# Performance work log

Hardware: AMD Instinct MI355X
Metric: run time of the kernel (lower is better)

Reference implementation:

```python
import jax, jax.numpy as jnp
import numpy as np

B, S, H, DH, DM = 1024, 32, 32, 32, 1024  # seq==heads==head_dim==32 forced by module's reshapes


def setup_inputs() -> dict:
    key = jax.random.key(0)
    k1, k2 = jax.random.split(key)
    x = jax.random.normal(k1, (B, S, DM), dtype=jnp.float32)
    mask = jnp.ones((1, 1, S, DH), dtype=bool)
    W_qkv = jax.random.normal(k2, (DM, 3 * H * DH), dtype=jnp.float32) / np.sqrt(DM).astype(np.float32)
    return {"x": x, "mask": mask, "W_qkv": W_qkv}


def _rope(t, sin, cos):
    # t: [B, S, H, DH]; sin/cos: [S] broadcast over the HEADS axis (axis 2), as in the original
    t1, t2 = jnp.split(t, 2, axis=-1)
    rot = jnp.concatenate([-t2, t1], axis=-1)
    return t * cos.reshape(1, 1, -1, 1) + rot * sin.reshape(1, 1, -1, 1)


def reference(x, mask, W_qkv):
    b, seq_len, _ = x.shape
    qkv = x @ W_qkv  # [B, S, 3*H*DH]
    q, k, v = jnp.split(qkv, 3, axis=-1)
    q = q.reshape(b, -1, H, DH)
    k = k.reshape(b, -1, H, DH)
    v = v.reshape(b, -1, H, DH)
    pos = jnp.arange(seq_len, dtype=x.dtype)
    sin, cos = jnp.sin(pos), jnp.cos(pos)
    q = _rope(q, sin, cos)
    k = _rope(k, sin, cos)
    # matmul over heads axis (faithful to original): [B,S,H,DH] @ [B,S,DH,H] -> [B,S,H,H]
    attn = jnp.matmul(q, k.transpose(0, 1, 3, 2)) / jnp.sqrt(jnp.asarray(DH, x.dtype))
    attn = attn.reshape(b, H, seq_len, DH)  # valid only because H == 32
    attn = jnp.where(jnp.broadcast_to(mask, attn.shape), attn, -jnp.inf)
    attn = jax.nn.softmax(attn, axis=-1)
    out = jnp.matmul(attn, v)  # [B,H,S,DH] @ [B,S,H,DH]; batched since S==H==32
    return out.reshape(-1, seq_len, H * DH)
```

## Files before the change

### kernel.cpp

```cpp
#include <hip/hip_runtime.h>

typedef __bf16 bf16_t;
typedef __bf16 bf16x4 __attribute__((ext_vector_type(4)));
typedef __bf16 bf16x8 __attribute__((ext_vector_type(8)));
typedef float f32x4 __attribute__((ext_vector_type(4)));
typedef float f32x16 __attribute__((ext_vector_type(16)));
typedef unsigned int uint4v __attribute__((ext_vector_type(4)));

#define M_TOT 32768
#define N_TOT 3072
#define K_TOT 1024

#define WT_BYTES (3072u * 1024u * 2u)
#define XB_BYTES ((size_t)M_TOT * 1024 * 2)

#define SLOT 32768

__device__ __forceinline__ void gload_lds16(const void* g, void* l) {
  __builtin_amdgcn_global_load_lds(
      (const __attribute__((address_space(1))) unsigned int*)g,
      (__attribute__((address_space(3))) unsigned int*)l, 16, 0, 0);
}

__device__ __forceinline__ unsigned pk2(float a, float b) {
  unsigned short lo = __builtin_bit_cast(unsigned short, (bf16_t)a);
  unsigned short hi = __builtin_bit_cast(unsigned short, (bf16_t)b);
  return ((unsigned)hi << 16) | (unsigned)lo;
}

__global__ __launch_bounds__(256) void k_wt(const float* __restrict__ W,
                                            bf16_t* __restrict__ wt) {
  __shared__ float tile[64][65];
  const int c0 = blockIdx.x * 64, k0 = blockIdx.y * 64;
  const int t = threadIdx.x;
  for (int rep = 0; rep < 16; ++rep) {
    int lin = rep * 256 + t;
    int kl = lin >> 6, cl = lin & 63;
    tile[kl][cl] = W[(size_t)(k0 + kl) * 3072 + (c0 + cl)];
  }
  __syncthreads();
  const float scale = 0.17677669529663687f;
  for (int rep = 0; rep < 16; ++rep) {
    int lin = rep * 256 + t;
    int cl = lin >> 6, kl = lin & 63;
    int c = c0 + cl;
    float val;
    if (c < 2048) {
      int cc = c & 1023;
      int h = cc >> 5, d = cc & 31;
      float cv = cosf((float)h), sv = sinf((float)h);
      int clp = cl + ((d < 16) ? 16 : -16);
      float other = tile[kl][clp];
      val = tile[kl][cl] * cv + ((d < 16) ? -other : other) * sv;
      if (c < 1024) val *= scale;
    } else {
      val = tile[kl][cl];
    }
    wt[(size_t)c * 1024 + (k0 + kl)] = (bf16_t)val;
  }
}

__global__ __launch_bounds__(256) void k_xb(const float* __restrict__ x,
                                            bf16_t* __restrict__ xb) {
  const size_t nf4 = (size_t)M_TOT * K_TOT / 4;
  const float4* src = (const float4*)x;
  for (size_t i = (size_t)blockIdx.x * 256 + threadIdx.x; i < nf4;
       i += (size_t)gridDim.x * 256) {
    float4 a = src[i];
    bf16x4 o;
    o[0] = (bf16_t)a.x; o[1] = (bf16_t)a.y; o[2] = (bf16_t)a.z; o[3] = (bf16_t)a.w;
    *(bf16x4*)(&xb[i * 4]) = o;
  }
}

template <int STAGE, int VM>
__device__ __forceinline__ void ktile(const char* sR, char* sW,
                                      const char* src, int dstOff,
                                      int aoff, int boff,
                                      f32x4 (&acc)[8][4]) {
  if constexpr (STAGE) {
#pragma unroll
    for (int c = 0; c < 4; ++c)
      gload_lds16(src + c * 32768, sW + dstOff + c * 1024);
  }
  bf16x8 a[8], b[4];
#pragma unroll
  for (int m = 0; m < 4; ++m) a[m] = *(const bf16x8*)(sR + aoff + m * 2048);
  b[0] = *(const bf16x8*)(sR + boff);
  b[1] = *(const bf16x8*)(sR + boff + 4096);
  __builtin_amdgcn_sched_barrier(0);
  b[2] = *(const bf16x8*)(sR + boff + 8192);
  b[3] = *(const bf16x8*)(sR + boff + 12288);
  __builtin_amdgcn_sched_barrier(0);
#pragma unroll
  for (int m = 4; m < 8; ++m) a[m] = *(const bf16x8*)(sR + aoff + m * 2048);
  __builtin_amdgcn_sched_barrier(0);

  asm volatile("s_waitcnt lgkmcnt(6)" ::: "memory");
  __builtin_amdgcn_sched_barrier(0);
  __builtin_amdgcn_s_setprio(1);
#pragma unroll
  for (int m = 0; m < 4; ++m)
#pragma unroll
    for (int n = 0; n < 2; ++n)
      acc[m][n] = __builtin_amdgcn_mfma_f32_16x16x32_bf16(a[m], b[n], acc[m][n], 0, 0, 0);
  __builtin_amdgcn_s_setprio(0);

  asm volatile("s_waitcnt lgkmcnt(4)" ::: "memory");
  __builtin_amdgcn_sched_barrier(0);
  __builtin_amdgcn_s_setprio(1);
#pragma unroll
  for (int m = 0; m < 4; ++m)
#pragma unroll
    for (int n = 2; n < 4; ++n)
      acc[m][n] = __builtin_amdgcn_mfma_f32_16x16x32_bf16(a[m], b[n], acc[m][n], 0, 0, 0);
  __builtin_amdgcn_s_setprio(0);

  asm volatile("s_waitcnt lgkmcnt(0)" ::: "memory");
  __builtin_amdgcn_sched_barrier(0);
  __builtin_amdgcn_s_setprio(1);
#pragma unroll
  for (int m = 4; m < 8; ++m)
#pragma unroll
    for (int n = 2; n < 4; ++n)
      acc[m][n] = __builtin_amdgcn_mfma_f32_16x16x32_bf16(a[m], b[n], acc[m][n], 0, 0, 0);
#pragma unroll
  for (int m = 4; m < 8; ++m)
#pragma unroll
    for (int n = 0; n < 2; ++n)
      acc[m][n] = __builtin_amdgcn_mfma_f32_16x16x32_bf16(a[m], b[n], acc[m][n], 0, 0, 0);
  __builtin_amdgcn_s_setprio(0);

  if constexpr (VM == 4) asm volatile("s_waitcnt vmcnt(4)" ::: "memory");
  else if constexpr (VM == 0) asm volatile("s_waitcnt vmcnt(0)" ::: "memory");
  if constexpr (VM >= 0) __builtin_amdgcn_s_barrier();
}

__global__ __launch_bounds__(512, 2) void k_gemm(const bf16_t* __restrict__ xb,
                                                 const bf16_t* __restrict__ wt,
                                                 bf16_t* __restrict__ qk,
                                                 bf16_t* __restrict__ vb) {
  __shared__ __attribute__((aligned(16))) char lds[3 * SLOT];
  const int tid = threadIdx.x;
  const int w = tid >> 6, lane = tid & 63;
  const int wr = w >> 2, wc = w & 3;

  const int bid = blockIdx.x;
  const int swz = (bid & 7) * 192 + (bid >> 3);
  const int tm = swz / 12, tn = swz % 12;
  const int row0 = tm * 256, col0 = tn * 256;

  const int isB = w >> 2;
  const int rL = (w & 3) * 64 + (lane >> 2);
  const int g = (lane & 3) ^ ((lane >> 3) & 3);
  const char* src = isB
      ? (const char*)wt + (size_t)(col0 + rL) * 2048 + g * 16
      : (const char*)xb + (size_t)(row0 + rL) * 2048 + g * 16;
  const int dstOff = (w & 3) * 4096 + isB * 16384;

  const int rsel = lane & 15;
  const int kx = (((lane >> 4) ^ ((rsel >> 1) & 3)) << 4);
  const int aoff = (wr * 16 + rsel) * 64 + kx;
  const int boff = 16384 + (wc * 16 + rsel) * 64 + kx;

  f32x4 acc[8][4];
#pragma unroll
  for (int m = 0; m < 8; ++m)
#pragma unroll
    for (int n = 0; n < 4; ++n)
#pragma unroll
      for (int i = 0; i < 4; ++i) acc[m][n][i] = 0.f;

  {
#pragma unroll
    for (int c = 0; c < 4; ++c) gload_lds16(src + c * 32768, lds + dstOff + c * 1024);
#pragma unroll
    for (int c = 0; c < 4; ++c) gload_lds16(src + 64 + c * 32768, lds + SLOT + dstOff + c * 1024);
    asm volatile("s_waitcnt vmcnt(4)" ::: "memory");
    __builtin_amdgcn_s_barrier();
  }

  const char* p = src + 128;
  for (int i = 0; i < 10; ++i) {
    ktile<1, 4>(lds,            lds + 2 * SLOT, p,       dstOff, aoff, boff, acc);
    ktile<1, 4>(lds + SLOT,     lds,            p + 64,  dstOff, aoff, boff, acc);
    ktile<1, 4>(lds + 2 * SLOT, lds + SLOT,     p + 128, dstOff, aoff, boff, acc);
    p += 192;
  }
  ktile<0, 0>(lds, lds, src, dstOff, aoff, boff, acc);
  ktile<0, -1>(lds + SLOT, lds, src, dstOff, aoff, boff, acc);

  const bool isv = (col0 >= 2048);
  const int rgrp = (lane >> 4) * 4;
#pragma unroll
  for (int m = 0; m < 8; ++m)
#pragma unroll
    for (int n = 0; n < 4; ++n)
#pragma unroll
      for (int reg = 0; reg < 4; ++reg) {
        const int R = row0 + wr * 16 + m * 32 + rgrp + reg;
        const int C = col0 + wc * 16 + n * 64 + rsel;
        const bf16_t val = (bf16_t)acc[m][n][reg];
        if (!isv) qk[(size_t)R * 2048 + C] = val;
        else      vb[(size_t)R * 1024 + (C - 2048)] = val;
      }
}

__global__ __launch_bounds__(256) void k_attn(const bf16_t* __restrict__ qk,
                                              const bf16_t* __restrict__ vb,
                                              float* __restrict__ out) {
  __shared__ __attribute__((aligned(16))) bf16_t vl[4][1024];
  const int t = threadIdx.x;
  const int w = t >> 6, lane = t & 63;
  const int r = blockIdx.x * 4 + w;
  const int jm = lane & 31, hi = lane >> 5;

  const char* vsrc = (const char*)vb + (size_t)r * 2048;
  gload_lds16(vsrc + lane * 16, (char*)vl[w]);
  gload_lds16(vsrc + 1024 + lane * 16, (char*)vl[w] + 1024);

  const char* rowbase = (const char*)qk + (size_t)r * 4096;
  const bf16x8 ak0 = *(const bf16x8*)(rowbase + 2048 + jm * 64 + hi * 16);
  const bf16x8 ak1 = *(const bf16x8*)(rowbase + 2048 + jm * 64 + 32 + hi * 16);
  const bf16x8 bq0 = *(const bf16x8*)(rowbase + jm * 64 + hi * 16);
  const bf16x8 bq1 = *(const bf16x8*)(rowbase + jm * 64 + 32 + hi * 16);

  f32x16 s;
  for (int i = 0; i < 16; ++i) s[i] = 0.f;
  s = __builtin_amdgcn_mfma_f32_32x32x16_bf16(ak0, bq0, s, 0, 0, 0);
  s = __builtin_amdgcn_mfma_f32_32x32x16_bf16(ak1, bq1, s, 0, 0, 0);

  float mx = s[0];
#pragma unroll
  for (int i = 1; i < 16; ++i) mx = fmaxf(mx, s[i]);
  mx = fmaxf(mx, __shfl_xor(mx, 32));
  float p[16];
  float sum = 0.f;
#pragma unroll
  for (int i = 0; i < 16; ++i) { p[i] = __expf(s[i] - mx); sum += p[i]; }
  sum += __shfl_xor(sum, 32);
  const float inv = 1.f / sum;
#pragma unroll
  for (int i = 0; i < 16; ++i) p[i] *= inv;

  const unsigned t01 = pk2(p[0], p[1]),  t23 = pk2(p[2], p[3]);
  const unsigned t45 = pk2(p[4], p[5]),  t67 = pk2(p[6], p[7]);
  const unsigned t89 = pk2(p[8], p[9]),  tab = pk2(p[10], p[11]);
  const unsigned tcd = pk2(p[12], p[13]), tef = pk2(p[14], p[15]);
  const unsigned x01 = (unsigned)__shfl_xor((int)t01, 32), x23 = (unsigned)__shfl_xor((int)t23, 32);
  const unsigned x45 = (unsigned)__shfl_xor((int)t45, 32), x67 = (unsigned)__shfl_xor((int)t67, 32);
  const unsigned x89 = (unsigned)__shfl_xor((int)t89, 32), xab = (unsigned)__shfl_xor((int)tab, 32);
  const unsigned xcd = (unsigned)__shfl_xor((int)tcd, 32), xef = (unsigned)__shfl_xor((int)tef, 32);
  uint4v u0, u1;
  u0[0] = hi ? x45 : t01; u0[1] = hi ? x67 : t23; u0[2] = hi ? t45 : x01; u0[3] = hi ? t67 : x23;
  u1[0] = hi ? xcd : t89; u1[1] = hi ? xef : tab; u1[2] = hi ? tcd : x89; u1[3] = hi ? tef : xab;
  const bf16x8 pa0 = __builtin_bit_cast(bf16x8, u0);
  const bf16x8 pa1 = __builtin_bit_cast(bf16x8, u1);

  asm volatile("s_waitcnt vmcnt(0)" ::: "memory");
  union { bf16x8 v; bf16_t e[8]; } v0, v1;
#pragma unroll
  for (int e = 0; e < 8; ++e) v0.e[e] = vl[w][(8 * hi + e) * 32 + jm];
#pragma unroll
  for (int e = 0; e < 8; ++e) v1.e[e] = vl[w][(16 + 8 * hi + e) * 32 + jm];

  f32x16 o;
  for (int i = 0; i < 16; ++i) o[i] = 0.f;
  o = __builtin_amdgcn_mfma_f32_32x32x16_bf16(pa0, v0.v, o, 0, 0, 0);
  o = __builtin_amdgcn_mfma_f32_32x32x16_bf16(pa1, v1.v, o, 0, 0, 0);

  float* orow = out + (size_t)r * 1024;
#pragma unroll
  for (int reg = 0; reg < 16; ++reg) {
    const int jrow = (reg & 3) + 8 * (reg >> 2) + 4 * hi;
    orow[jrow * 32 + jm] = o[reg];
  }
}

extern "C" void kernel_launch(void* const* d_in, const int* in_sizes, int n_in,
                              void* d_out, int out_size, void* d_ws, size_t ws_size,
                              hipStream_t stream) {
  const float* x = (const float*)d_in[0];
  const float* W = (const float*)d_in[2];

  char* ws = (char*)d_ws;
  bf16_t* wt = (bf16_t*)ws;
  bf16_t* xb = (bf16_t*)(ws + WT_BYTES);
  bf16_t* vb = (bf16_t*)(ws + WT_BYTES + XB_BYTES);

  k_wt <<<dim3(48, 16), 256, 0, stream>>>(W, wt);
  k_xb <<<16384, 256, 0, stream>>>(x, xb);
  k_gemm<<<1536, 512, 0, stream>>>(xb, wt, (bf16_t*)d_out, vb);
  k_attn<<<8192, 256, 0, stream>>>((const bf16_t*)d_out, vb, (float*)d_out);
}
```

Before: 305.9 us.

## Merge prep kernels and software-pipeline LDS fragment loads across K-tiles in GEMM

Folds the weight-transpose/RoPE kernel and the x-to-bf16 cast kernel into one launch, split by block index. It also restructures the GEMM main loop so the next tile's A and B fragments are prefetched from LDS into registers while the current tile's second half of MFMAs runs. Global-to-LDS copies are split around the MFMA groups, and launch bounds drop to one block per CU. The aim is to hide LDS latency and cut one launch, at the cost of extra registers and possibly lower occupancy.

```diff
diff --git a/kernel.cpp b/kernel.cpp
--- a/kernel.cpp
+++ b/kernel.cpp
@@ -28,115 +28,103 @@
   return ((unsigned)hi << 16) | (unsigned)lo;
 }
 
-__global__ __launch_bounds__(256) void k_wt(const float* __restrict__ W,
-                                            bf16_t* __restrict__ wt) {
-  __shared__ float tile[64][65];
-  const int c0 = blockIdx.x * 64, k0 = blockIdx.y * 64;
+__global__ __launch_bounds__(256) void k_prep(const float* __restrict__ x,
+                                              const float* __restrict__ W,
+                                              bf16_t* __restrict__ xb,
+                                              bf16_t* __restrict__ wt) {
+  const int bid = blockIdx.x;
   const int t = threadIdx.x;
-  for (int rep = 0; rep < 16; ++rep) {
-    int lin = rep * 256 + t;
-    int kl = lin >> 6, cl = lin & 63;
-    tile[kl][cl] = W[(size_t)(k0 + kl) * 3072 + (c0 + cl)];
-  }
-  __syncthreads();
-  const float scale = 0.17677669529663687f;
-  for (int rep = 0; rep < 16; ++rep) {
-    int lin = rep * 256 + t;
-    int cl = lin >> 6, kl = lin & 63;
-    int c = c0 + cl;
-    float val;
-    if (c < 2048) {
-      int cc = c & 1023;
-      int h = cc >> 5, d = cc & 31;
-      float cv = cosf((float)h), sv = sinf((float)h);
-      int clp = cl + ((d < 16) ? 16 : -16);
-      float other = tile[kl][clp];
-      val = tile[kl][cl] * cv + ((d < 16) ? -other : other) * sv;
-      if (c < 1024) val *= scale;
-    } else {
-      val = tile[kl][cl];
+  if (bid < 768) {
+    __shared__ float tile[64][65];
+    const int c0 = (bid % 48) * 64, k0 = (bid / 48) * 64;
+    for (int rep = 0; rep < 16; ++rep) {
+      int lin = rep * 256 + t;
+      int kl = lin >> 6, cl = lin & 63;
+      tile[kl][cl] = W[(size_t)(k0 + kl) * 3072 + (c0 + cl)];
     }
-    wt[(size_t)c * 1024 + (k0 + kl)] = (bf16_t)val;
-  }
-}
-
-__global__ __launch_bounds__(256) void k_xb(const float* __restrict__ x,
-                                            bf16_t* __restrict__ xb) {
-  const size_t nf4 = (size_t)M_TOT * K_TOT / 4;
-  const float4* src = (const float4*)x;
-  for (size_t i = (size_t)blockIdx.x * 256 + threadIdx.x; i < nf4;
-       i += (size_t)gridDim.x * 256) {
-    float4 a = src[i];
-    bf16x4 o;
-    o[0] = (bf16_t)a.x; o[1] = (bf16_t)a.y; o[2] = (bf16_t)a.z; o[3] = (bf16_t)a.w;
-    *(bf16x4*)(&xb[i * 4]) = o;
-  }
-}
-
-template <int STAGE, int VM>
-__device__ __forceinline__ void ktile(const char* sR, char* sW,
-                                      const char* src, int dstOff,
-                                      int aoff, int boff,
-                                      f32x4 (&acc)[8][4]) {
-  if constexpr (STAGE) {
-#pragma unroll
-    for (int c = 0; c < 4; ++c)
-      gload_lds16(src + c * 32768, sW + dstOff + c * 1024);
-  }
-  bf16x8 a[8], b[4];
-#pragma unroll
-  for (int m = 0; m < 4; ++m) a[m] = *(const bf16x8*)(sR + aoff + m * 2048);
-  b[0] = *(const bf16x8*)(sR + boff);
-  b[1] = *(const bf16x8*)(sR + boff + 4096);
-  __builtin_amdgcn_sched_barrier(0);
-  b[2] = *(const bf16x8*)(sR + boff + 8192);
-  b[3] = *(const bf16x8*)(sR + boff + 12288);
-  __builtin_amdgcn_sched_barrier(0);
-#pragma unroll
-  for (int m = 4; m < 8; ++m) a[m] = *(const bf16x8*)(sR + aoff + m * 2048);
-  __builtin_amdgcn_sched_barrier(0);
-
-  asm volatile("s_waitcnt lgkmcnt(6)" ::: "memory");
-  __builtin_amdgcn_sched_barrier(0);
-  __builtin_amdgcn_s_setprio(1);
-#pragma unroll
-  for (int m = 0; m < 4; ++m)
-#pragma unroll
-    for (int n = 0; n < 2; ++n)
-      acc[m][n] = __builtin_amdgcn_mfma_f32_16x16x32_bf16(a[m], b[n], acc[m][n], 0, 0, 0);
-  __builtin_amdgcn_s_setprio(0);
-
+    __syncthreads();
+    const float scale = 0.17677669529663687f;
+    for (int rep = 0; rep < 16; ++rep) {
+      int lin = rep * 256 + t;
+      int cl = lin >> 6, kl = lin & 63;
+      int c = c0 + cl;
+      float val;
+      if (c < 2048) {
+        int cc = c & 1023;
+        int h = cc >> 5, d = cc & 31;
+        float cv = cosf((float)h), sv = sinf((float)h);
+        int clp = cl + ((d < 16) ? 16 : -16);
+        float other = tile[kl][clp];
+        val = tile[kl][cl] * cv + ((d < 16) ? -other : other) * sv;
+        if (c < 1024) val *= scale;
+      } else {
+        val = tile[kl][cl];
+      }
+      wt[(size_t)c * 1024 + (k0 + kl)] = (bf16_t)val;
+    }
+  } else {
+    const size_t nf4 = (size_t)M_TOT * K_TOT / 4;
+    const float4* src = (const float4*)x;
+    for (size_t i = (size_t)(bid - 768) * 256 + t; i < nf4; i += (size_t)16384 * 256) {
+      float4 a = src[i];
+      bf16x4 o;
+      o[0] = (bf16_t)a.x; o[1] = (bf16_t)a.y; o[2] = (bf16_t)a.z; o[3] = (bf16_t)a.w;
+      *(bf16x4*)(&xb[i * 4]) = o;
+    }
+  }
+}
+
+template <int STG>
+__device__ __forceinline__ void kt(const char* sR, const char* sN, char* sW,
+                                   const char* pS, int dstOff,
+                                   int aoff, int boff,
+                                   f32x4 (&acc)[8][4],
+                                   bf16x8 (&aQ1)[4], bf16x8 (&bC)[4],
+                                   bf16x8 (&bN)[4]) {
+  bf16x8 aQ2[4];
+  if constexpr (STG == 1) {
+    gload_lds16(pS, sW + dstOff);
+    gload_lds16(pS + 32768, sW + dstOff + 1024);
+  }
+#pragma unroll
+  for (int i = 0; i < 4; ++i)
+    aQ2[i] = *(const bf16x8*)(sR + aoff + (4 + i) * 2048);
   asm volatile("s_waitcnt lgkmcnt(4)" ::: "memory");
   __builtin_amdgcn_sched_barrier(0);
   __builtin_amdgcn_s_setprio(1);
 #pragma unroll
   for (int m = 0; m < 4; ++m)
 #pragma unroll
-    for (int n = 2; n < 4; ++n)
-      acc[m][n] = __builtin_amdgcn_mfma_f32_16x16x32_bf16(a[m], b[n], acc[m][n], 0, 0, 0);
+    for (int n = 0; n < 4; ++n)
+      acc[m][n] = __builtin_amdgcn_mfma_f32_16x16x32_bf16(aQ1[m], bC[n], acc[m][n], 0, 0, 0);
   __builtin_amdgcn_s_setprio(0);
-
+  if constexpr (STG == 1) {
+    gload_lds16(pS + 65536, sW + dstOff + 2048);
+    gload_lds16(pS + 98304, sW + dstOff + 3072);
+    asm volatile("s_waitcnt vmcnt(4)" ::: "memory");
+  } else if constexpr (STG == 2) {
+    asm volatile("s_waitcnt vmcnt(0)" ::: "memory");
+  }
   asm volatile("s_waitcnt lgkmcnt(0)" ::: "memory");
   __builtin_amdgcn_sched_barrier(0);
+  if constexpr (STG <= 2) {
+    __builtin_amdgcn_s_barrier();
+#pragma unroll
+    for (int i = 0; i < 4; ++i) aQ1[i] = *(const bf16x8*)(sN + aoff + i * 2048);
+#pragma unroll
+    for (int i = 0; i < 4; ++i) bN[i] = *(const bf16x8*)(sN + boff + i * 4096);
+    __builtin_amdgcn_sched_barrier(0);
+  }
   __builtin_amdgcn_s_setprio(1);
 #pragma unroll
-  for (int m = 4; m < 8; ++m)
-#pragma unroll
-    for (int n = 2; n < 4; ++n)
-      acc[m][n] = __builtin_amdgcn_mfma_f32_16x16x32_bf16(a[m], b[n], acc[m][n], 0, 0, 0);
-#pragma unroll
-  for (int m = 4; m < 8; ++m)
-#pragma unroll
-    for (int n = 0; n < 2; ++n)
-      acc[m][n] = __builtin_amdgcn_mfma_f32_16x16x32_bf16(a[m], b[n], acc[m][n], 0, 0, 0);
+  for (int m = 0; m < 4; ++m)
+#pragma unroll
+    for (int n = 0; n < 4; ++n)
+      acc[m + 4][n] = __builtin_amdgcn_mfma_f32_16x16x32_bf16(aQ2[m], bC[n], acc[m + 4][n], 0, 0, 0);
   __builtin_amdgcn_s_setprio(0);
-
-  if constexpr (VM == 4) asm volatile("s_waitcnt vmcnt(4)" ::: "memory");
-  else if constexpr (VM == 0) asm volatile("s_waitcnt vmcnt(0)" ::: "memory");
-  if constexpr (VM >= 0) __builtin_amdgcn_s_barrier();
-}
-
-__global__ __launch_bounds__(512, 2) void k_gemm(const bf16_t* __restrict__ xb,
+}
+
+__global__ __launch_bounds__(512, 1) void k_gemm(const bf16_t* __restrict__ xb,
                                                  const bf16_t* __restrict__ wt,
                                                  bf16_t* __restrict__ qk,
                                                  bf16_t* __restrict__ vb) {
@@ -158,8 +146,8 @@
       : (const char*)xb + (size_t)(row0 + rL) * 2048 + g * 16;
   const int dstOff = (w & 3) * 4096 + isB * 16384;
 
-  const int rsel = lane & 15;
-  const int kx = (((lane >> 4) ^ ((rsel >> 1) & 3)) << 4);
+  const int rsel = lane & 15, kslot = lane >> 4;
+  const int kx = ((kslot ^ ((rsel >> 1) & 3)) << 4);
   const int aoff = (wr * 16 + rsel) * 64 + kx;
   const int boff = 16384 + (wc * 16 + rsel) * 64 + kx;
 
@@ -171,27 +159,41 @@
 #pragma unroll
       for (int i = 0; i < 4; ++i) acc[m][n][i] = 0.f;
 
+  bf16x8 aQ1[4], bX[4], bY[4];
+
+  char* const S0 = lds;
+  char* const S1 = lds + SLOT;
+  char* const S2 = lds + 2 * SLOT;
+
   {
 #pragma unroll
-    for (int c = 0; c < 4; ++c) gload_lds16(src + c * 32768, lds + dstOff + c * 1024);
-#pragma unroll
-    for (int c = 0; c < 4; ++c) gload_lds16(src + 64 + c * 32768, lds + SLOT + dstOff + c * 1024);
+    for (int c = 0; c < 4; ++c) gload_lds16(src + c * 32768, S0 + dstOff + c * 1024);
+#pragma unroll
+    for (int c = 0; c < 4; ++c) gload_lds16(src + 64 + c * 32768, S1 + dstOff + c * 1024);
     asm volatile("s_waitcnt vmcnt(4)" ::: "memory");
     __builtin_amdgcn_s_barrier();
-  }
-
-  const char* p = src + 128;
-  for (int i = 0; i < 10; ++i) {
-    ktile<1, 4>(lds,            lds + 2 * SLOT, p,       dstOff, aoff, boff, acc);
-    ktile<1, 4>(lds + SLOT,     lds,            p + 64,  dstOff, aoff, boff, acc);
-    ktile<1, 4>(lds + 2 * SLOT, lds + SLOT,     p + 128, dstOff, aoff, boff, acc);
-    p += 192;
-  }
-  ktile<0, 0>(lds, lds, src, dstOff, aoff, boff, acc);
-  ktile<0, -1>(lds + SLOT, lds, src, dstOff, aoff, boff, acc);
+    __builtin_amdgcn_sched_barrier(0);
+#pragma unroll
+    for (int i = 0; i < 4; ++i) aQ1[i] = *(const bf16x8*)(S0 + aoff + i * 2048);
+#pragma unroll
+    for (int i = 0; i < 4; ++i) bX[i] = *(const bf16x8*)(S0 + boff + i * 4096);
+  }
+
+  const char* pS = src + 128;
+  for (int i = 0; i < 5; ++i) {
+    kt<1>(S0, S1, S2, pS,       dstOff, aoff, boff, acc, aQ1, bX, bY);
+    kt<1>(S1, S2, S0, pS + 64,  dstOff, aoff, boff, acc, aQ1, bY, bX);
+    kt<1>(S2, S0, S1, pS + 128, dstOff, aoff, boff, acc, aQ1, bX, bY);
+    kt<1>(S0, S1, S2, pS + 192, dstOff, aoff, boff, acc, aQ1, bY, bX);
+    kt<1>(S1, S2, S0, pS + 256, dstOff, aoff, boff, acc, aQ1, bX, bY);
+    kt<1>(S2, S0, S1, pS + 320, dstOff, aoff, boff, acc, aQ1, bY, bX);
+    pS += 384;
+  }
+  kt<2>(S0, S1, S2, pS, dstOff, aoff, boff, acc, aQ1, bX, bY);
+  kt<3>(S1, S1, S2, pS, dstOff, aoff, boff, acc, aQ1, bY, bX);
 
   const bool isv = (col0 >= 2048);
-  const int rgrp = (lane >> 4) * 4;
+  const int rgrp = kslot * 4;
 #pragma unroll
   for (int m = 0; m < 8; ++m)
 #pragma unroll
@@ -288,8 +290,7 @@
   bf16_t* xb = (bf16_t*)(ws + WT_BYTES);
   bf16_t* vb = (bf16_t*)(ws + WT_BYTES + XB_BYTES);
 
-  k_wt <<<dim3(48, 16), 256, 0, stream>>>(W, wt);
-  k_xb <<<16384, 256, 0, stream>>>(x, xb);
+  k_prep<<<17152, 256, 0, stream>>>(x, W, xb, wt);
   k_gemm<<<1536, 512, 0, stream>>>(xb, wt, (bf16_t*)d_out, vb);
   k_attn<<<8192, 256, 0, stream>>>((const bf16_t*)d_out, vb, (float*)d_out);
 }
```

Measured after the change: 290.2 us, median of 2. -5.1%, faster.
